# Optimization experiments

Hardware: AMD Instinct MI355X
Metric: run time of the kernel (lower is better)

## Reference

```python
import jax, jax.numpy as jnp
import numpy as np

N_PTS = 100000
C_IN, C_OUT, K = 16, 32, 3
B, D, H, W = 2, 32, 128, 128


def setup_inputs() -> dict:
    key = jax.random.key(0)
    kf, kw, kb, kz, ky, kx = jax.random.split(key, 6)
    features = jax.random.normal(kf, (N_PTS, C_IN), dtype=jnp.float32)
    coords = jnp.stack([
        jax.random.randint(kb, (N_PTS,), 0, B),
        jax.random.randint(kz, (N_PTS,), 0, D),
        jax.random.randint(ky, (N_PTS,), 0, H),
        jax.random.randint(kx, (N_PTS,), 0, W),
    ], axis=1).astype(jnp.int32)
    weight = jax.random.normal(kw, (K ** 3, C_IN, C_OUT), dtype=jnp.float32) * 0.01
    bias = jnp.zeros((C_OUT,), dtype=jnp.float32)
    return {"features": features, "coords": coords, "weight": weight, "bias": bias,
            "batch_size": B, "d_sp": D, "h_sp": H, "w_sp": W}


def reference(features, coords, weight, bias, batch_size, d_sp, h_sp, w_sp):
    # Scatter sparse voxel features into dense grid (B, C_in, D, H, W).
    n, c_in = features.shape
    c_out = weight.shape[2]
    k = K
    b, z, y, x = coords[:, 0], coords[:, 1], coords[:, 2], coords[:, 3]
    dense = jnp.zeros((batch_size, c_in, d_sp, h_sp, w_sp), dtype=features.dtype)
    dense = dense.at[b, :, z, y, x].set(features)  # (N,) advanced idx -> rows of (N, C_in)
    # Conv3d: torch copies weight.view(C_out, C_in, k, k, k) -> OIDHW kernel.
    kernel = weight.reshape(c_out, c_in, k, k, k)
    out = jax.lax.conv_general_dilated(
        dense, kernel,
        window_strides=(1, 1, 1),
        padding=[(1, 1), (1, 1), (1, 1)],
        dimension_numbers=("NCDHW", "OIDHW", "NCDHW"))
    out = jax.nn.relu(out + bias[None, :, None, None, None])
    # Dense equivalent of the torch nonzero-gather (which has data-dependent
    # shape): return the full dense activated grid (B, C_out, D, H, W).
    return out
```

## Files before the change

### kernel.cpp

```cpp
#include <hip/hip_runtime.h>

#define CIN   16
#define COUT  32
#define BATCH 2
#define DSP   32
#define HSP   128
#define WSP   128
#define NVOX  (BATCH*DSP*HSP*WSP)

#define DP (DSP+2)
#define HP (HSP+2)
#define WP (WSP+2)
#define ZSTR (HP*WP)
#define NVOXP (BATCH*DP*HP*WP)

#define TZ 4
#define TY 8
#define TX 32
#define PZ 6
#define PYY 10
#define PXX 34
#define PROW (PYY*PXX)
#define PVOX (PZ*PROW)
#define NCHUNK (2*PVOX)
#define NCHPAD 4096
#define NPAIR 14
#define NWREP ((NPAIR*2*64*8 + 255)/256)
#define FILLT (NVOXP*CIN/8)
#define NFILL ((FILLT + 255)/256)

typedef __bf16 bf16x8 __attribute__((ext_vector_type(8)));
typedef float  f32x4  __attribute__((ext_vector_type(4)));

__device__ __forceinline__ void load_lds16(const void* g, void* l) {
    __builtin_amdgcn_global_load_lds(
        (const __attribute__((address_space(1))) unsigned*)g,
        (__attribute__((address_space(3))) unsigned*)l, 16, 0, 0);
}

__global__ void k_prep(const int4* __restrict__ coords, int n, int nbDedup,
                       int* __restrict__ map,
                       const float* __restrict__ w, __bf16* __restrict__ wpack,
                       uint4* __restrict__ dense4) {
    int bb = blockIdx.x;
    if (bb < nbDedup) {
        int p = bb * 256 + threadIdx.x;
        if (p >= n) return;
        int4 c = coords[p];
        int vox = ((c.x*DSP + c.y)*HSP + c.z)*WSP + c.w;
        atomicMax(&map[vox], p);
    } else if (bb < nbDedup + NWREP) {
        int i = (bb - nbDedup) * 256 + threadIdx.x;
        if (i >= NPAIR*2*64*8) return;
        int j = i & 7, l = (i>>3) & 63, h = (i>>9) & 1, p = i >> 10;
        int tap = 2*p + ((l>>4)>>1);
        int co  = h*16 + (l & 15);
        int ci  = ((l>>4)&1)*8 + j;
        float v = (tap < 27) ? w[(co*CIN + ci)*27 + tap] : 0.0f;
        wpack[i] = (__bf16)v;
    } else {
        int i = (bb - nbDedup - NWREP) * 256 + threadIdx.x;
        if (i < FILLT) dense4[i] = make_uint4(0,0,0,0);
    }
}

__global__ void k_scatter(const int4* __restrict__ coords, const int* __restrict__ map,
                          const float* __restrict__ feat, __bf16* __restrict__ dense,
                          int n) {
    int p = blockIdx.x * 256 + threadIdx.x;
    if (p >= n) return;
    int4 c = coords[p];
    int vox = ((c.x*DSP + c.y)*HSP + c.z)*WSP + c.w;
    if (map[vox] != p) return;
    const float4* fp = (const float4*)(feat + (size_t)p*CIN);
    float4 f0 = fp[0], f1 = fp[1], f2 = fp[2], f3 = fp[3];
    bf16x8 lo = { (__bf16)f0.x,(__bf16)f0.y,(__bf16)f0.z,(__bf16)f0.w,
                  (__bf16)f1.x,(__bf16)f1.y,(__bf16)f1.z,(__bf16)f1.w };
    bf16x8 hi = { (__bf16)f2.x,(__bf16)f2.y,(__bf16)f2.z,(__bf16)f2.w,
                  (__bf16)f3.x,(__bf16)f3.y,(__bf16)f3.z,(__bf16)f3.w };
    size_t voxp = (((size_t)c.x*DP + (c.y+1))*HP + (c.z+1))*WP + (c.w+1);
    __bf16* d = dense + voxp*CIN;
    *(bf16x8*)d       = lo;
    *(bf16x8*)(d + 8) = hi;
}

__device__ __forceinline__ void stage_tile(const __bf16* __restrict__ gb,
                                           ushort* lbase, int wave, int lane) {
    #pragma unroll
    for (int it = 0; it < 8; ++it) {
        int j0 = wave*64 + it*512;
        int j  = j0 + lane;
        int jj = j < NCHUNK ? j : NCHUNK-1;
        int h  = (jj >= PVOX) ? 1 : 0;
        int v  = jj - h*PVOX;
        int pz = v / PROW;
        int rem = v - pz*PROW;
        int py = rem / PXX;
        int px = rem - py*PXX;
        load_lds16(gb + ((size_t)(pz*ZSTR + py*WP + px))*CIN + h*8,
                   (void*)(lbase + (size_t)j0*8));
    }
}

__global__ __launch_bounds__(512, 2) void k_conv(
    const __bf16* __restrict__ dense, const __bf16* __restrict__ wpack,
    const float* __restrict__ bias, float* __restrict__ out)
{
    __shared__ __align__(16) ushort patch[2][NCHPAD*8];

    int bid = blockIdx.x;
    int bs  = (bid & 7) * 32 + (bid >> 3);
    int tyi = bs & 15, tzi = (bs >> 4) & 7, b = bs >> 7;
    int z0 = tzi*TZ, y0 = tyi*TY;

    int tid  = threadIdx.x;
    int lane = tid & 63, wave = tid >> 6;
    int lx16  = lane & 15;
    int lhalf = (lane >> 4) & 1;
    int ltp   = (lane >> 4) >> 1;
    int zw    = wave >> 1;
    int yb    = (wave & 1) * 4;

    int voff[NPAIR];
    #pragma unroll
    for (int p = 0; p < NPAIR; ++p) {
        int tap = 2*p + ltp; if (tap > 26) tap = 26;
        int kd = tap/9, kh = (tap/3)%3, kw = tap%3;
        voff[p] = (kd*PYY + kh)*PXX + kw;
    }
    float bv0 = bias[lx16], bv1 = bias[16 + lx16];

    bf16x8 wf[NPAIR][2];
    #pragma unroll
    for (int p = 0; p < NPAIR; ++p)
        #pragma unroll
        for (int h = 0; h < 2; ++h)
            wf[p][h] = *(const bf16x8*)(wpack + (size_t)((p*2 + h)*64 + lane)*8);

    const __bf16* grow = dense + ((((size_t)b*DP + z0)*HP + y0)*WP)*CIN;

    stage_tile(grow, patch[0], wave, lane);

    #pragma unroll 1
    for (int t = 0; t < 4; ++t) {
        if (t < 3) {
            stage_tile(grow + (size_t)(t+1)*TX*CIN, patch[(t+1)&1], wave, lane);
            asm volatile("s_waitcnt vmcnt(8)\ns_barrier" ::: "memory");
        } else {
            asm volatile("s_waitcnt vmcnt(0)\ns_barrier" ::: "memory");
        }
        __builtin_amdgcn_sched_barrier(0);

        f32x4 acc[8][2];
        #pragma unroll
        for (int gi = 0; gi < 8; ++gi) {
            acc[gi][0] = (f32x4){0.f,0.f,0.f,0.f};
            acc[gi][1] = (f32x4){0.f,0.f,0.f,0.f};
        }
        const ushort* pb = patch[t&1] +
            ((size_t)lhalf*PVOX + (zw*PYY + yb)*PXX + lx16)*8;
        #pragma unroll
        for (int p = 0; p < NPAIR; ++p) {
            const ushort* pa = pb + (size_t)voff[p]*8;
            #pragma unroll
            for (int gi = 0; gi < 8; ++gi) {
                bf16x8 a = *(const bf16x8*)(pa + ((gi>>1)*PXX + (gi&1)*16)*8);
                acc[gi][0] = __builtin_amdgcn_mfma_f32_16x16x32_bf16(a, wf[p][0], acc[gi][0], 0,0,0);
                acc[gi][1] = __builtin_amdgcn_mfma_f32_16x16x32_bf16(a, wf[p][1], acc[gi][1], 0,0,0);
            }
        }

        asm volatile("s_barrier" ::: "memory");
        __builtin_amdgcn_sched_barrier(0);

        #pragma unroll
        for (int gi = 0; gi < 8; ++gi) {
            int y = yb + (gi >> 1), xg = gi & 1;
            int gz = z0 + zw, gy = y0 + y;
            int gx = t*TX + xg*16 + ((lane >> 4) << 2);
            f32x4 o0, o1;
            o0[0] = fmaxf(acc[gi][0][0]+bv0, 0.f); o0[1] = fmaxf(acc[gi][0][1]+bv0, 0.f);
            o0[2] = fmaxf(acc[gi][0][2]+bv0, 0.f); o0[3] = fmaxf(acc[gi][0][3]+bv0, 0.f);
            o1[0] = fmaxf(acc[gi][1][0]+bv1, 0.f); o1[1] = fmaxf(acc[gi][1][1]+bv1, 0.f);
            o1[2] = fmaxf(acc[gi][1][2]+bv1, 0.f); o1[3] = fmaxf(acc[gi][1][3]+bv1, 0.f);
            size_t base0 = ((((size_t)b*COUT + lx16)*DSP + gz)*HSP + gy)*WSP + gx;
            size_t base1 = base0 + (size_t)16*DSP*HSP*WSP;
            *(f32x4*)(out + base0) = o0;
            *(f32x4*)(out + base1) = o1;
        }
    }
}

extern "C" void kernel_launch(void* const* d_in, const int* in_sizes, int n_in,
                              void* d_out, int out_size, void* d_ws, size_t ws_size,
                              hipStream_t stream) {
    const float* feat   = (const float*)d_in[0];
    const int4*  coords = (const int4*)d_in[1];
    const float* weight = (const float*)d_in[2];
    const float* bias   = (const float*)d_in[3];
    float* out = (float*)d_out;
    int n = in_sizes[0] / CIN;

    int*    map   = (int*)d_ws;
    __bf16* dense = (__bf16*)(map + NVOX);
    __bf16* wpack = dense + (size_t)NVOXP*CIN;

    hipMemsetAsync(map, 0xFF, (size_t)NVOX*sizeof(int), stream);

    int nb = (n + 255) / 256;
    k_prep   <<<nb + NWREP + NFILL, 256, 0, stream>>>(coords, n, nb, map, weight,
                                                      wpack, (uint4*)dense);
    k_scatter<<<nb, 256, 0, stream>>>(coords, map, feat, dense, n);
    k_conv   <<<256, 512, 0, stream>>>(dense, wpack, bias, out);
}
```

Baseline: 82.66 us.

## Gather dense grid in one fill pass and relax conv vmcnt waits

```diff
diff --git a/kernel.cpp b/kernel.cpp
--- a/kernel.cpp
+++ b/kernel.cpp
@@ -13,6 +13,7 @@
 #define WP (WSP+2)
 #define ZSTR (HP*WP)
 #define NVOXP (BATCH*DP*HP*WP)
+#define NDCH  (NVOXP*2)
 
 #define TZ 4
 #define TY 8
@@ -26,8 +27,6 @@
 #define NCHPAD 4096
 #define NPAIR 14
 #define NWREP ((NPAIR*2*64*8 + 255)/256)
-#define FILLT (NVOXP*CIN/8)
-#define NFILL ((FILLT + 255)/256)
 
 typedef __bf16 bf16x8 __attribute__((ext_vector_type(8)));
 typedef float  f32x4  __attribute__((ext_vector_type(4)));
@@ -40,8 +39,7 @@
 
 __global__ void k_prep(const int4* __restrict__ coords, int n, int nbDedup,
                        int* __restrict__ map,
-                       const float* __restrict__ w, __bf16* __restrict__ wpack,
-                       uint4* __restrict__ dense4) {
+                       const float* __restrict__ w, __bf16* __restrict__ wpack) {
     int bb = blockIdx.x;
     if (bb < nbDedup) {
         int p = bb * 256 + threadIdx.x;
@@ -49,7 +47,7 @@
         int4 c = coords[p];
         int vox = ((c.x*DSP + c.y)*HSP + c.z)*WSP + c.w;
         atomicMax(&map[vox], p);
-    } else if (bb < nbDedup + NWREP) {
+    } else {
         int i = (bb - nbDedup) * 256 + threadIdx.x;
         if (i >= NPAIR*2*64*8) return;
         int j = i & 7, l = (i>>3) & 63, h = (i>>9) & 1, p = i >> 10;
@@ -58,30 +56,32 @@
         int ci  = ((l>>4)&1)*8 + j;
         float v = (tap < 27) ? w[(co*CIN + ci)*27 + tap] : 0.0f;
         wpack[i] = (__bf16)v;
-    } else {
-        int i = (bb - nbDedup - NWREP) * 256 + threadIdx.x;
-        if (i < FILLT) dense4[i] = make_uint4(0,0,0,0);
-    }
-}
-
-__global__ void k_scatter(const int4* __restrict__ coords, const int* __restrict__ map,
-                          const float* __restrict__ feat, __bf16* __restrict__ dense,
-                          int n) {
-    int p = blockIdx.x * 256 + threadIdx.x;
-    if (p >= n) return;
-    int4 c = coords[p];
-    int vox = ((c.x*DSP + c.y)*HSP + c.z)*WSP + c.w;
-    if (map[vox] != p) return;
-    const float4* fp = (const float4*)(feat + (size_t)p*CIN);
-    float4 f0 = fp[0], f1 = fp[1], f2 = fp[2], f3 = fp[3];
-    bf16x8 lo = { (__bf16)f0.x,(__bf16)f0.y,(__bf16)f0.z,(__bf16)f0.w,
-                  (__bf16)f1.x,(__bf16)f1.y,(__bf16)f1.z,(__bf16)f1.w };
-    bf16x8 hi = { (__bf16)f2.x,(__bf16)f2.y,(__bf16)f2.z,(__bf16)f2.w,
-                  (__bf16)f3.x,(__bf16)f3.y,(__bf16)f3.z,(__bf16)f3.w };
-    size_t voxp = (((size_t)c.x*DP + (c.y+1))*HP + (c.z+1))*WP + (c.w+1);
-    __bf16* d = dense + voxp*CIN;
-    *(bf16x8*)d       = lo;
-    *(bf16x8*)(d + 8) = hi;
+    }
+}
+
+__global__ void k_fill(const int* __restrict__ map, const float* __restrict__ feat,
+                       __bf16* __restrict__ dense) {
+    int c = blockIdx.x * 256 + threadIdx.x;
+    if (c >= NDCH) return;
+    int v = c >> 1, h = c & 1;
+    int bb = v / (DP*ZSTR);
+    int r  = v - bb*(DP*ZSTR);
+    int zp = r / ZSTR;  r -= zp*ZSTR;
+    int yp = r / WP;
+    int xp = r - yp*WP;
+    bf16x8 val = { (__bf16)0.f,(__bf16)0.f,(__bf16)0.f,(__bf16)0.f,
+                   (__bf16)0.f,(__bf16)0.f,(__bf16)0.f,(__bf16)0.f };
+    if ((unsigned)(zp-1) < DSP && (unsigned)(yp-1) < HSP && (unsigned)(xp-1) < WSP) {
+        int vox = ((bb*DSP + (zp-1))*HSP + (yp-1))*WSP + (xp-1);
+        int p = map[vox];
+        if (p >= 0) {
+            const float4* fp = (const float4*)(feat + (size_t)p*CIN) + h*2;
+            float4 f0 = fp[0], f1 = fp[1];
+            val = bf16x8{ (__bf16)f0.x,(__bf16)f0.y,(__bf16)f0.z,(__bf16)f0.w,
+                          (__bf16)f1.x,(__bf16)f1.y,(__bf16)f1.z,(__bf16)f1.w };
+        }
+    }
+    *(bf16x8*)(dense + (size_t)v*CIN + h*8) = val;
 }
 
 __device__ __forceinline__ void stage_tile(const __bf16* __restrict__ gb,
@@ -143,12 +143,10 @@
 
     #pragma unroll 1
     for (int t = 0; t < 4; ++t) {
-        if (t < 3) {
-            stage_tile(grow + (size_t)(t+1)*TX*CIN, patch[(t+1)&1], wave, lane);
-            asm volatile("s_waitcnt vmcnt(8)\ns_barrier" ::: "memory");
-        } else {
-            asm volatile("s_waitcnt vmcnt(0)\ns_barrier" ::: "memory");
-        }
+        if (t < 3) stage_tile(grow + (size_t)(t+1)*TX*CIN, patch[(t+1)&1], wave, lane);
+        if (t == 0)      asm volatile("s_waitcnt vmcnt(8)\ns_barrier"  ::: "memory");
+        else if (t < 3)  asm volatile("s_waitcnt vmcnt(24)\ns_barrier" ::: "memory");
+        else             asm volatile("s_waitcnt vmcnt(16)\ns_barrier" ::: "memory");
         __builtin_amdgcn_sched_barrier(0);
 
         f32x4 acc[8][2];
@@ -208,8 +206,7 @@
     hipMemsetAsync(map, 0xFF, (size_t)NVOX*sizeof(int), stream);
 
     int nb = (n + 255) / 256;
-    k_prep   <<<nb + NWREP + NFILL, 256, 0, stream>>>(coords, n, nb, map, weight,
-                                                      wpack, (uint4*)dense);
-    k_scatter<<<nb, 256, 0, stream>>>(coords, map, feat, dense, n);
-    k_conv   <<<256, 512, 0, stream>>>(dense, wpack, bias, out);
-}
+    k_prep<<<nb + NWREP, 256, 0, stream>>>(coords, n, nb, map, weight, wpack);
+    k_fill<<<(NDCH + 255)/256, 256, 0, stream>>>(map, feat, dense);
+    k_conv<<<256, 512, 0, stream>>>(dense, wpack, bias, out);
+}
```

Result: faster. 73.41 us (-11.2%).
